# Performance work log

Measured on AMD Instinct MI355X. Metric: run time of the kernel, lower is better.

The kernel has to match this reference:

```python
import jax, jax.numpy as jnp
import numpy as np

NUM_FERNS = 16
K_BITS = 10          # bits per fern -> table size 2^K = 1024
NUM_ACTIVE = 8       # A active words per pixel
LP = 3               # log2(NUM_ACTIVE) ambiguous bits
D_OUT = 64


def setup_inputs() -> dict:
    key = jax.random.key(0)
    k1, k2 = jax.random.split(key)
    # bit-function activations in [0,1]: probability that each bit is 1
    B = jax.random.uniform(k1, (64, NUM_FERNS * K_BITS, 32, 32), dtype=jnp.float32)
    # per-fern vote tables: rows indexed by the K-bit hash word
    tables = jax.random.normal(k2, (NUM_FERNS, 2 ** K_BITS, D_OUT), dtype=jnp.float32) * 0.02
    return {"B": B, "tables": tables}


def _fern(T, table):
    # T: [N, K, H, W] bit probabilities for one fern; table: [2^K, d_out]
    N, K, H, W = T.shape
    # hard bits and base word code (first bit is MSB, matching the shift-or loop)
    bits = jnp.round(T).astype(jnp.int32)
    shifts = (K - 1 - jnp.arange(K, dtype=jnp.int32))[None, :, None, None]
    WB = jnp.sum(jnp.left_shift(bits, shifts), axis=1)            # [N,H,W]
    ba = jnp.abs(T - 0.5)                                         # bit ambiguity
    a_bits = jnp.arange(NUM_ACTIVE, dtype=jnp.int32)              # [A]
    IT = jnp.broadcast_to(WB[:, None], (N, NUM_ACTIVE, H, W))     # active word codes
    AT = jnp.ones((N, NUM_ACTIVE, H, W), dtype=T.dtype)           # active word weights
    for j in range(LP):
        idx = jnp.argmin(ba, axis=1)                              # [N,H,W] most ambiguous bit
        p1 = jnp.take_along_axis(T, idx[:, None], axis=1)[:, 0]   # [N,H,W] P(bit=1)
        ba = ba + jax.nn.one_hot(idx, K, axis=1, dtype=ba.dtype)  # exclude chosen bit
        shift = (K - 1 - idx)[:, None]                            # [N,1,H,W]
        mask = jnp.left_shift(jnp.int32(1), shift)
        bit_j = ((a_bits >> j) & 1)[None, :, None, None]          # [1,A,1,1]
        IT = jnp.where(bit_j == 1, IT | mask, IT & ~mask)
        AT = AT * jnp.where(bit_j == 1, p1[:, None], 1.0 - p1[:, None])
    votes = table[IT]                                             # gather: [N,A,H,W,d_out]
    return jnp.einsum('nahw,nahwd->nhwd', AT, votes)              # [N,H,W,d_out]


def reference(B, tables):
    N, C, H, W = B.shape
    T = B.reshape(N, NUM_FERNS, K_BITS, H, W)
    per_fern = jax.vmap(_fern, in_axes=(1, 0))(T, tables)         # [M,N,H,W,d_out]
    return jnp.sum(per_fern, axis=0)
```

## Files before the change

### kernel.cpp

```cpp
#include <hip/hip_runtime.h>


#define NFERN 16
#define KBITS 10

__global__ __launch_bounds__(256, 4)
void fern_kernel(const float* __restrict__ B,
                 const float* __restrict__ tables,
                 float* __restrict__ out) {
    const int t  = (int)threadIdx.x;
    const int s  = t & 3;
    const int pl = t >> 2;
    const int pixel = (int)blockIdx.x * 64 + pl;
    const int n  = pixel >> 10;
    const int hw = pixel & 1023;

    const float* bptr = B + (size_t)n * (NFERN * KBITS * 1024) + hw;

    float4 acc[4];
    #pragma unroll
    for (int j = 0; j < 4; ++j) acc[j] = make_float4(0.f, 0.f, 0.f, 0.f);

    #pragma unroll 1
    for (int m = 0; m < NFERN; ++m) {
        float tk[KBITS];
        #pragma unroll
        for (int k = 0; k < KBITS; ++k)
            tk[k] = bptr[(m * KBITS + k) * 1024];

        unsigned wb = 0u;
        float ba[KBITS];
        #pragma unroll
        for (int k = 0; k < KBITS; ++k) {
            wb = (wb << 1) | (tk[k] > 0.5f ? 1u : 0u);
            ba[k] = fabsf(tk[k] - 0.5f);
        }

        int i0, i1, i2;
        float p0, p1, p2;
        {
            float bv = 1e30f; int bi = 0; float bpv = 0.f;
            #pragma unroll
            for (int k = 0; k < KBITS; ++k) {
                bool c = ba[k] < bv;
                bv  = c ? ba[k] : bv;
                bi  = c ? k      : bi;
                bpv = c ? tk[k]  : bpv;
            }
            i0 = bi; p0 = bpv;
        }
        {
            float bv = 1e30f; int bi = 0; float bpv = 0.f;
            #pragma unroll
            for (int k = 0; k < KBITS; ++k) {
                float v = (k == i0) ? 1e30f : ba[k];
                bool c = v < bv;
                bv  = c ? v     : bv;
                bi  = c ? k     : bi;
                bpv = c ? tk[k] : bpv;
            }
            i1 = bi; p1 = bpv;
        }
        {
            float bv = 1e30f; int bi = 0; float bpv = 0.f;
            #pragma unroll
            for (int k = 0; k < KBITS; ++k) {
                float v = (k == i0 || k == i1) ? 1e30f : ba[k];
                bool c = v < bv;
                bv  = c ? v     : bv;
                bi  = c ? k     : bi;
                bpv = c ? tk[k] : bpv;
            }
            i2 = bi; p2 = bpv;
        }

        const unsigned m0 = 1u << (KBITS - 1 - i0);
        const unsigned m1 = 1u << (KBITS - 1 - i1);
        const unsigned m2 = 1u << (KBITS - 1 - i2);
        const float q0 = 1.f - p0, q1 = 1.f - p1, q2 = 1.f - p2;

        const float* tabm = tables + (size_t)m * (1024 * 64) + s * 4;

        #pragma unroll
        for (int a = 0; a < 8; ++a) {
            unsigned it = wb;
            float at = 1.f;
            if (a & 1) { it |= m0; at *= p0; } else { it &= ~m0; at *= q0; }
            if (a & 2) { it |= m1; at *= p1; } else { it &= ~m1; at *= q1; }
            if (a & 4) { it |= m2; at *= p2; } else { it &= ~m2; at *= q2; }
            const float* row = tabm + (size_t)it * 64;
            #pragma unroll
            for (int j = 0; j < 4; ++j) {
                float4 v = *(const float4*)(row + j * 16);
                acc[j].x = fmaf(at, v.x, acc[j].x);
                acc[j].y = fmaf(at, v.y, acc[j].y);
                acc[j].z = fmaf(at, v.z, acc[j].z);
                acc[j].w = fmaf(at, v.w, acc[j].w);
            }
        }
    }

    float* op = out + (size_t)pixel * 64 + s * 4;
    #pragma unroll
    for (int j = 0; j < 4; ++j)
        *(float4*)(op + j * 16) = acc[j];
}

extern "C" void kernel_launch(void* const* d_in, const int* in_sizes, int n_in,
                              void* d_out, int out_size, void* d_ws, size_t ws_size,
                              hipStream_t stream) {
    const float* B      = (const float*)d_in[0];
    const float* tables = (const float*)d_in[1];
    float* out          = (float*)d_out;
    fern_kernel<<<dim3(1024), dim3(256), 0, stream>>>(B, tables, out);
}
```

Baseline: 165.7 us.

## Stage per-fern table slices in LDS with async double buffering, split output dims

Reorganizes the work so each block handles 1024 pixels and an 8-wide slice of the output dimension. Each fern's 1024x8 table slice is copied into LDS with global_load_lds and double-buffered, so the random row gathers hit LDS instead of global memory/L2. An XOR swizzle on the two 16-byte halves aims to reduce bank conflicts. The cost is that every block recomputes the hash and ambiguous-bit selection, and the B reads are repeated eight times across the dq blocks. It also adds a barrier per fern, and the 1024-thread blocks use 64KB of LDS.

```diff
diff --git a/kernel.cpp b/kernel.cpp
--- a/kernel.cpp
+++ b/kernel.cpp
@@ -4,37 +4,66 @@
 #define NFERN 16
 #define KBITS 10
 
-__global__ __launch_bounds__(256, 4)
+typedef __attribute__((address_space(1))) const void GV;
+typedef __attribute__((address_space(3))) void LV;
+__device__ __forceinline__ void g2lds16(const void* g, void* l) {
+    __builtin_amdgcn_global_load_lds((GV*)g, (LV*)l, 16u, 0, 0u);
+}
+
+__global__ __launch_bounds__(1024, 8)
 void fern_kernel(const float* __restrict__ B,
                  const float* __restrict__ tables,
                  float* __restrict__ out) {
-    const int t  = (int)threadIdx.x;
-    const int s  = t & 3;
-    const int pl = t >> 2;
-    const int pixel = (int)blockIdx.x * 64 + pl;
-    const int n  = pixel >> 10;
-    const int hw = pixel & 1023;
+    __shared__ __align__(16) float lds[2][1024 * 8];
 
-    const float* bptr = B + (size_t)n * (NFERN * KBITS * 1024) + hw;
+    const int t   = (int)threadIdx.x;
+    const int bid = (int)blockIdx.x;
+    const int pg  = bid & 63;
+    const int dq  = bid >> 6;
+    const int pixel = pg * 1024 + t;
 
-    float4 acc[4];
-    #pragma unroll
-    for (int j = 0; j < 4; ++j) acc[j] = make_float4(0.f, 0.f, 0.f, 0.f);
+    const float* bptr = B + (size_t)pg * (NFERN * KBITS * 1024) + t;
+    const float* tq   = tables + dq * 8;
+
+    const int st_sl = (t & 1) ^ ((t >> 3) & 1);
+
+    float4 acc0 = make_float4(0.f, 0.f, 0.f, 0.f);
+    float4 acc1 = make_float4(0.f, 0.f, 0.f, 0.f);
+
+    {
+        const float* base = tq;
+        #pragma unroll
+        for (int R = 0; R < 2; ++R) {
+            const int r = R * 512 + (t >> 1);
+            g2lds16(base + (size_t)r * 64 + st_sl * 4,
+                    (char*)(&lds[0][0]) + R * 16384 + t * 16);
+        }
+    }
+    __syncthreads();
 
     #pragma unroll 1
     for (int m = 0; m < NFERN; ++m) {
+        if (m + 1 < NFERN) {
+            const float* base = tq + (size_t)(m + 1) * (1024 * 64);
+            const int buf = (m + 1) & 1;
+            #pragma unroll
+            for (int R = 0; R < 2; ++R) {
+                const int r = R * 512 + (t >> 1);
+                g2lds16(base + (size_t)r * 64 + st_sl * 4,
+                        (char*)(&lds[buf][0]) + R * 16384 + t * 16);
+            }
+        }
+        const float* L = &lds[m & 1][0];
+
         float tk[KBITS];
         #pragma unroll
         for (int k = 0; k < KBITS; ++k)
             tk[k] = bptr[(m * KBITS + k) * 1024];
 
         unsigned wb = 0u;
-        float ba[KBITS];
         #pragma unroll
-        for (int k = 0; k < KBITS; ++k) {
+        for (int k = 0; k < KBITS; ++k)
             wb = (wb << 1) | (tk[k] > 0.5f ? 1u : 0u);
-            ba[k] = fabsf(tk[k] - 0.5f);
-        }
 
         int i0, i1, i2;
         float p0, p1, p2;
@@ -42,10 +71,9 @@
             float bv = 1e30f; int bi = 0; float bpv = 0.f;
             #pragma unroll
             for (int k = 0; k < KBITS; ++k) {
-                bool c = ba[k] < bv;
-                bv  = c ? ba[k] : bv;
-                bi  = c ? k      : bi;
-                bpv = c ? tk[k]  : bpv;
+                float v = fabsf(tk[k] - 0.5f);
+                bool c = v < bv;
+                bv = c ? v : bv;  bi = c ? k : bi;  bpv = c ? tk[k] : bpv;
             }
             i0 = bi; p0 = bpv;
         }
@@ -53,11 +81,9 @@
             float bv = 1e30f; int bi = 0; float bpv = 0.f;
             #pragma unroll
             for (int k = 0; k < KBITS; ++k) {
-                float v = (k == i0) ? 1e30f : ba[k];
+                float v = (k == i0) ? 1e30f : fabsf(tk[k] - 0.5f);
                 bool c = v < bv;
-                bv  = c ? v     : bv;
-                bi  = c ? k     : bi;
-                bpv = c ? tk[k] : bpv;
+                bv = c ? v : bv;  bi = c ? k : bi;  bpv = c ? tk[k] : bpv;
             }
             i1 = bi; p1 = bpv;
         }
@@ -65,11 +91,9 @@
             float bv = 1e30f; int bi = 0; float bpv = 0.f;
             #pragma unroll
             for (int k = 0; k < KBITS; ++k) {
-                float v = (k == i0 || k == i1) ? 1e30f : ba[k];
+                float v = (k == i0 || k == i1) ? 1e30f : fabsf(tk[k] - 0.5f);
                 bool c = v < bv;
-                bv  = c ? v     : bv;
-                bi  = c ? k     : bi;
-                bpv = c ? tk[k] : bpv;
+                bv = c ? v : bv;  bi = c ? k : bi;  bpv = c ? tk[k] : bpv;
             }
             i2 = bi; p2 = bpv;
         }
@@ -79,8 +103,6 @@
         const unsigned m2 = 1u << (KBITS - 1 - i2);
         const float q0 = 1.f - p0, q1 = 1.f - p1, q2 = 1.f - p2;
 
-        const float* tabm = tables + (size_t)m * (1024 * 64) + s * 4;
-
         #pragma unroll
         for (int a = 0; a < 8; ++a) {
             unsigned it = wb;
@@ -88,22 +110,26 @@
             if (a & 1) { it |= m0; at *= p0; } else { it &= ~m0; at *= q0; }
             if (a & 2) { it |= m1; at *= p1; } else { it &= ~m1; at *= q1; }
             if (a & 4) { it |= m2; at *= p2; } else { it &= ~m2; at *= q2; }
-            const float* row = tabm + (size_t)it * 64;
-            #pragma unroll
-            for (int j = 0; j < 4; ++j) {
-                float4 v = *(const float4*)(row + j * 16);
-                acc[j].x = fmaf(at, v.x, acc[j].x);
-                acc[j].y = fmaf(at, v.y, acc[j].y);
-                acc[j].z = fmaf(at, v.z, acc[j].z);
-                acc[j].w = fmaf(at, v.w, acc[j].w);
-            }
+            const int   bswz = (int)((it >> 2) & 1u);
+            const float* rowp = L + it * 8;
+            float4 v0 = *(const float4*)(rowp + bswz * 4);
+            float4 v1 = *(const float4*)(rowp + (1 ^ bswz) * 4);
+            acc0.x = fmaf(at, v0.x, acc0.x);
+            acc0.y = fmaf(at, v0.y, acc0.y);
+            acc0.z = fmaf(at, v0.z, acc0.z);
+            acc0.w = fmaf(at, v0.w, acc0.w);
+            acc1.x = fmaf(at, v1.x, acc1.x);
+            acc1.y = fmaf(at, v1.y, acc1.y);
+            acc1.z = fmaf(at, v1.z, acc1.z);
+            acc1.w = fmaf(at, v1.w, acc1.w);
         }
+
+        __syncthreads();
     }
 
-    float* op = out + (size_t)pixel * 64 + s * 4;
-    #pragma unroll
-    for (int j = 0; j < 4; ++j)
-        *(float4*)(op + j * 16) = acc[j];
+    float* op = out + (size_t)pixel * 64 + dq * 8;
+    *(float4*)op       = acc0;
+    *(float4*)(op + 4) = acc1;
 }
 
 extern "C" void kernel_launch(void* const* d_in, const int* in_sizes, int n_in,
@@ -112,5 +138,5 @@
     const float* B      = (const float*)d_in[0];
     const float* tables = (const float*)d_in[1];
     float* out          = (float*)d_out;
-    fern_kernel<<<dim3(1024), dim3(256), 0, stream>>>(B, tables, out);
+    fern_kernel<<<dim3(512), dim3(1024), 0, stream>>>(B, tables, out);
 }
```

New measurement: 179.1 us. 8.1% more time.
